# Performance work log

Measured on AMD Instinct MI355X. Metric: run time of the kernel, lower is better.

The kernel has to match this reference:

```python
import jax, jax.numpy as jnp
import numpy as np
from jax import lax

C, NH, HC, HID, P = 192, 8, 64, 512, 16
B, H, W = 2, 128, 128
EPS = 1e-5


def setup_inputs() -> dict:
    key = jax.random.key(0)
    ks = jax.random.split(key, 12)
    f = lambda i, shape: jax.random.normal(ks[i], shape, jnp.float32) * 0.05
    return dict(
        x=jax.random.normal(ks[0], (B, C, H, W), jnp.float32),
        ln1_g=jnp.ones((C,), jnp.float32), ln1_b=jnp.zeros((C,), jnp.float32),
        wq=f(1, (HID, C)), wk=f(2, (HID, C)), wv=f(3, (HID, C)),
        wo=f(4, (C, HID)), bo=jnp.zeros((C,), jnp.float32),
        dw_w=f(5, (C, 1, 3, 3)), dw_b=jnp.zeros((C,), jnp.float32),
        mlp_w=f(6, (C, 2 * C)), mlp_b=jnp.zeros((C,), jnp.float32),
        ln2_g=jnp.ones((C,), jnp.float32), ln2_b=jnp.zeros((C,), jnp.float32),
        c1_w=f(7, (C, C)), c1_b=jnp.zeros((C,), jnp.float32),
        res_w=f(8, (C, 1, 3, 3)), res_b=jnp.zeros((C,), jnp.float32),
        c2_w=f(9, (C, C)), c2_b=jnp.zeros((C,), jnp.float32),
    )


def ln_ch(x, g, b):
    # LayerNorm over the channel dim of an NCHW tensor (biased variance, like torch)
    m = x.mean(1, keepdims=True)
    v = ((x - m) ** 2).mean(1, keepdims=True)
    return (x - m) / jnp.sqrt(v + EPS) * g[None, :, None, None] + b[None, :, None, None]


def inorm(x):
    # InstanceNorm2d, affine=False
    m = x.mean((2, 3), keepdims=True)
    v = ((x - m) ** 2).mean((2, 3), keepdims=True)
    return (x - m) / jnp.sqrt(v + EPS)


def conv1x1(x, w, b=None):
    y = jnp.einsum('oc,bchw->bohw', w, x)
    return y if b is None else y + b[None, :, None, None]


def dwconv(x, w, b):
    y = lax.conv_general_dilated(x, w, (1, 1), 'SAME',
                                 feature_group_count=x.shape[1],
                                 dimension_numbers=('NCHW', 'OIHW', 'NCHW'))
    return y + b[None, :, None, None]


def res_block(x, w, b):
    return jax.nn.gelu(inorm(dwconv(x, w, b)), approximate=False) + x


def dpsa(x, ln_g, ln_b, wq, wk, wv, wo, bo):
    Bs, _, Hs, Ws = x.shape
    xn = ln_ch(x, ln_g, ln_b)

    def proj(w):  # -> (B*NH, H, W, HC)
        t = jnp.einsum('oc,bchw->bohw', w, xn)
        return t.reshape(Bs * NH, HC, Hs, Ws).transpose(0, 2, 3, 1)

    l2n = lambda t: t / jnp.maximum(jnp.linalg.norm(t, axis=-1, keepdims=True), 1e-12)
    q = l2n(proj(wq))
    k = l2n(proj(wk))
    v = proj(wv)

    qs = q.sum((1, 2))                                   # (BH, HC)
    h_scores = jnp.einsum('bc,bhc->bh', qs, k.sum(2))    # (BH, H)
    w_scores = jnp.einsum('bc,bwc->bw', qs, k.sum(1))    # (BH, W)
    _, h_idx = lax.top_k(h_scores, P)
    _, w_idx = lax.top_k(w_scores, P)

    k = jnp.take_along_axis(k, h_idx[:, :, None, None], axis=1)   # (BH, P, W, HC)
    v = jnp.take_along_axis(v, h_idx[:, :, None, None], axis=1)
    k = jnp.take_along_axis(k, w_idx[:, None, :, None], axis=2)   # (BH, P, P, HC)
    v = jnp.take_along_axis(v, w_idx[:, None, :, None], axis=2)

    qf = q.reshape(Bs * NH, Hs * Ws, HC)
    kf = k.reshape(Bs * NH, P * P, HC)
    vf = v.reshape(Bs * NH, P * P, HC)
    attn = jax.nn.softmax(jnp.einsum('bqc,bkc->bqk', qf, kf), axis=-1)
    out = jnp.einsum('bqk,bkc->bqc', attn, vf)
    out = out.reshape(Bs, NH, Hs, Ws, HC).transpose(0, 1, 4, 2, 3).reshape(Bs, NH * HC, Hs, Ws)
    return conv1x1(out, wo, bo)


def reference(x, ln1_g, ln1_b, wq, wk, wv, wo, bo, dw_w, dw_b, mlp_w, mlp_b,
              ln2_g, ln2_b, c1_w, c1_b, res_w, res_b, c2_w, c2_b):
    global_branch = dpsa(x, ln1_g, ln1_b, wq, wk, wv, wo, bo)
    local_branch = dwconv(x, dw_w, dw_b)
    f = jnp.concatenate((local_branch, global_branch), axis=1)
    f = conv1x1(f, mlp_w, mlp_b) + x
    y = ln_ch(f, ln2_g, ln2_b)
    y = jax.nn.gelu(inorm(conv1x1(y, c1_w, c1_b)), approximate=False)
    y = res_block(y, res_w, res_b)
    y = inorm(conv1x1(y, c2_w, c2_b))
    return y
```

## Files before the change

### kernel.cpp

```cpp
#include <hip/hip_runtime.h>
#include <math.h>

constexpr int kC   = 192;
constexpr int kNH  = 8;
constexpr int kHC  = 64;
constexpr int kHID = 512;
constexpr int kP   = 16;
constexpr int kB   = 2;
constexpr int kH   = 128;
constexpr int kW   = 128;
constexpr int kHW  = kH * kW;
constexpr int kN   = kB * kHW;
constexpr float kEPS = 1e-5f;

typedef __attribute__((ext_vector_type(8))) short bf16x8;
typedef __attribute__((ext_vector_type(4))) float f32x4;

__device__ inline unsigned short f2bf(float f) {
    unsigned int u = __builtin_bit_cast(unsigned int, f);
    unsigned int r = (u + 0x7FFFu + ((u >> 16) & 1u)) >> 16;
    return (unsigned short)r;
}
__device__ inline float bf2f(unsigned short u) {
    return __builtin_bit_cast(float, (unsigned int)u << 16);
}
__device__ inline unsigned int cvtpk(float lo, float hi) {
    unsigned int r;
    asm("v_cvt_pk_bf16_f32 %0, %1, %2" : "=v"(r) : "v"(lo), "v"(hi));
    return r;
}
__device__ inline unsigned long long pk4(float a, float b, float c, float d) {
    return (unsigned long long)cvtpk(a, b) | ((unsigned long long)cvtpk(c, d) << 32);
}
__device__ inline f32x4 ubf4(unsigned long long u) {
    f32x4 r;
    r[0] = bf2f((unsigned short)u);
    r[1] = bf2f((unsigned short)(u >> 16));
    r[2] = bf2f((unsigned short)(u >> 32));
    r[3] = bf2f((unsigned short)(u >> 48));
    return r;
}
__device__ inline float gelu_f(float x) {
    return 0.5f * x * (1.0f + erff(x * 0.70710678118654752f));
}

__global__ void prep_kernel(float* __restrict__ zbase,
                            const float* wq, const float* wk, const float* wm,
                            const float* c1, const float* c2,
                            const float* wo, const float* mlp_b, const float* bo,
                            unsigned short* wqb, unsigned short* wkb,
                            unsigned short* mlpb1, unsigned short* c1b, unsigned short* c2b,
                            unsigned short* w2pb, float* bp2)
{
    int i = blockIdx.x * 256 + threadIdx.x;
    if (i < 2304) { zbase[i] = 0.f; return; }
    i -= 2304;
    if (i < 98304) { wqb[i] = f2bf(wq[i]); return; }
    i -= 98304;
    if (i < 98304) { wkb[i] = f2bf(wk[i]); return; }
    i -= 98304;
    if (i < 36864) { int o = i / 192, k = i - o * 192; mlpb1[i] = f2bf(wm[o * 384 + k]); return; }
    i -= 36864;
    if (i < 36864) { c1b[i] = f2bf(c1[i]); return; }
    i -= 36864;
    if (i < 36864) { c2b[i] = f2bf(c2[i]); return; }
    i -= 36864;
    if (i < 98304) {
        int o = i >> 9, j = i & 511;
        const float* a = wm + o * 384 + 192;
        float s = 0.f;
        for (int c = 0; c < 192; ++c) s += a[c] * wo[c * 512 + j];
        w2pb[o * 512 + j] = f2bf(s);
        if (j == 0) {
            float t = mlp_b[o];
            for (int c = 0; c < 192; ++c) t += a[c] * bo[c];
            bp2[o] = t;
        }
    }
}

__global__ __launch_bounds__(256) void txln_kernel(const float* __restrict__ x,
                                                   unsigned short* __restrict__ xpb,
                                                   unsigned short* __restrict__ xnb,
                                                   const float* __restrict__ g,
                                                   const float* __restrict__ bb)
{
    __shared__ float tile[192][65];
    __shared__ float red[2][4][64];
    __shared__ float pms[64], prs[64];
    int hw0 = blockIdx.x * 64;
    int b   = blockIdx.y;
    int tid = threadIdx.x;
    for (int i = tid; i < 192 * 64; i += 256) {
        int c = i >> 6, p = i & 63;
        tile[c][p] = x[(size_t)(b * kC + c) * kHW + hw0 + p];
    }
    __syncthreads();
    {
        int p = tid & 63, qt = tid >> 6;
        float s = 0.f, ss = 0.f;
        for (int c = qt * 48; c < qt * 48 + 48; ++c) {
            float v = tile[c][p]; s += v; ss += v * v;
        }
        red[0][qt][p] = s; red[1][qt][p] = ss;
    }
    __syncthreads();
    if (tid < 64) {
        float s  = red[0][0][tid] + red[0][1][tid] + red[0][2][tid] + red[0][3][tid];
        float ss = red[1][0][tid] + red[1][1][tid] + red[1][2][tid] + red[1][3][tid];
        float m = s * (1.0f / kC);
        float var = ss * (1.0f / kC) - m * m;
        pms[tid] = m;
        prs[tid] = rsqrtf(var + kEPS);
    }
    __syncthreads();
    for (int i = tid; i < 64 * 192; i += 256) {
        int p = i / 192, c = i - p * 192;
        float raw = tile[c][p];
        size_t oi = (size_t)(b * kHW + hw0 + p) * kC + c;
        xpb[oi] = f2bf(raw);
        xnb[oi] = f2bf((raw - pms[p]) * prs[p] * g[c] + bb[c]);
    }
}

__global__ void ln_pm_bf16_kernel(const unsigned short* __restrict__ in,
                                  unsigned short* __restrict__ out,
                                  const float* __restrict__ g, const float* __restrict__ bb)
{
    int t = blockIdx.x * 256 + threadIdx.x;
    int n = t >> 2, q = t & 3;
    const unsigned long long* ip = (const unsigned long long*)(in + (size_t)n * kC) + q * 12;
    f32x4 v[12];
    float s = 0.f, ss = 0.f;
#pragma unroll
    for (int r = 0; r < 12; ++r) {
        v[r] = ubf4(ip[r]);
        s  += (v[r][0] + v[r][1]) + (v[r][2] + v[r][3]);
        ss += (v[r][0]*v[r][0] + v[r][1]*v[r][1]) + (v[r][2]*v[r][2] + v[r][3]*v[r][3]);
    }
    s  += __shfl_xor(s, 1);  s  += __shfl_xor(s, 2);
    ss += __shfl_xor(ss, 1); ss += __shfl_xor(ss, 2);
    float m  = s * (1.0f / kC);
    float var = ss * (1.0f / kC) - m * m;
    float rs = rsqrtf(var + kEPS);
    unsigned long long* op = (unsigned long long*)(out + (size_t)n * kC) + q * 12;
#pragma unroll
    for (int r = 0; r < 12; ++r) {
        f32x4 gg = *(const f32x4*)(g + q * 48 + r * 4);
        f32x4 bv = *(const f32x4*)(bb + q * 48 + r * 4);
        op[r] = pk4((v[r][0]-m)*rs*gg[0] + bv[0], (v[r][1]-m)*rs*gg[1] + bv[1],
                    (v[r][2]-m)*rs*gg[2] + bv[2], (v[r][3]-m)*rs*gg[3] + bv[3]);
    }
}

#define MGEMM_CORE(KVAL, APTR, BPTR)                                              \
    {                                                                             \
        const unsigned short* Ap = APTR;                                          \
        const unsigned short* Bp = BPTR;                                          \
        _Pragma("unroll 2")                                                       \
        for (int k = 0; k < KVAL; k += 32) {                                      \
            bf16x8 a0 = *(const bf16x8*)(Ap + k);                                 \
            bf16x8 a1 = *(const bf16x8*)(Ap + (size_t)16 * KVAL + k);             \
            bf16x8 b0 = *(const bf16x8*)(Bp + k);                                 \
            bf16x8 b1 = *(const bf16x8*)(Bp + (size_t)16 * KVAL + k);             \
            bf16x8 b2 = *(const bf16x8*)(Bp + (size_t)32 * KVAL + k);             \
            bf16x8 b3 = *(const bf16x8*)(Bp + (size_t)48 * KVAL + k);             \
            acc[0][0] = __builtin_amdgcn_mfma_f32_16x16x32_bf16(a0, b0, acc[0][0], 0, 0, 0); \
            acc[0][1] = __builtin_amdgcn_mfma_f32_16x16x32_bf16(a0, b1, acc[0][1], 0, 0, 0); \
            acc[0][2] = __builtin_amdgcn_mfma_f32_16x16x32_bf16(a0, b2, acc[0][2], 0, 0, 0); \
            acc[0][3] = __builtin_amdgcn_mfma_f32_16x16x32_bf16(a0, b3, acc[0][3], 0, 0, 0); \
            acc[1][0] = __builtin_amdgcn_mfma_f32_16x16x32_bf16(a1, b0, acc[1][0], 0, 0, 0); \
            acc[1][1] = __builtin_amdgcn_mfma_f32_16x16x32_bf16(a1, b1, acc[1][1], 0, 0, 0); \
            acc[1][2] = __builtin_amdgcn_mfma_f32_16x16x32_bf16(a1, b2, acc[1][2], 0, 0, 0); \
            acc[1][3] = __builtin_amdgcn_mfma_f32_16x16x32_bf16(a1, b3, acc[1][3], 0, 0, 0); \
        }                                                                         \
    }

__global__ __launch_bounds__(256) void qk_proj_kernel(
    const unsigned short* __restrict__ wqb, const unsigned short* __restrict__ wkb,
    const unsigned short* __restrict__ xnb,
    unsigned short* __restrict__ qpb, unsigned short* __restrict__ kpb,
    float* __restrict__ qpart, float* __restrict__ ksum_h)
{
    __shared__ float rbuf[2][2][4][4][4];
    int nB = blockIdx.x * 128;
    int hp = blockIdx.y;
    const unsigned short* A = blockIdx.z ? wkb : wqb;
    unsigned short* out = blockIdx.z ? kpb : qpb;
    float* red_out = blockIdx.z ? ksum_h : qpart;

    int w = threadIdx.x >> 6, lane = threadIdx.x & 63;
    int l15 = lane & 15, g = lane >> 4;
    int wm = w & 1, wn = w >> 1;
    int oB = hp * 128;

    const unsigned short* Ap = A + (size_t)(oB + wm * 64 + l15) * 192 + 8 * g;
    const unsigned short* Bp = xnb + (size_t)(nB + wn * 64 + l15) * 192 + 8 * g;

    f32x4 acc[4][4];
#pragma unroll
    for (int mt = 0; mt < 4; ++mt)
#pragma unroll
        for (int nt = 0; nt < 4; ++nt) acc[mt][nt] = (f32x4){0.f,0.f,0.f,0.f};

#pragma unroll 2
    for (int k = 0; k < 192; k += 32) {
        bf16x8 a[4], bb[4];
#pragma unroll
        for (int mt = 0; mt < 4; ++mt) a[mt] = *(const bf16x8*)(Ap + (size_t)mt * 16 * 192 + k);
#pragma unroll
        for (int nt = 0; nt < 4; ++nt) bb[nt] = *(const bf16x8*)(Bp + (size_t)nt * 16 * 192 + k);
#pragma unroll
        for (int mt = 0; mt < 4; ++mt)
#pragma unroll
            for (int nt = 0; nt < 4; ++nt)
                acc[mt][nt] = __builtin_amdgcn_mfma_f32_16x16x32_bf16(a[mt], bb[nt], acc[mt][nt], 0, 0, 0);
    }

    float sc[4];
#pragma unroll
    for (int nt = 0; nt < 4; ++nt) {
        float s = 0.f;
#pragma unroll
        for (int mt = 0; mt < 4; ++mt) {
            f32x4 a = acc[mt][nt];
            s += (a[0]*a[0] + a[1]*a[1]) + (a[2]*a[2] + a[3]*a[3]);
        }
        s += __shfl_xor(s, 16);
        s += __shfl_xor(s, 32);
        sc[nt] = 1.0f / fmaxf(sqrtf(s), 1e-12f);
    }

#pragma unroll
    for (int nt = 0; nt < 4; ++nt) {
        int n = nB + wn * 64 + nt * 16 + l15;
#pragma unroll
        for (int mt = 0; mt < 4; ++mt) {
            int o = oB + wm * 64 + mt * 16 + 4 * g;
            f32x4 v = acc[mt][nt];
            *(unsigned long long*)(out + (size_t)n * kHID + o) =
                pk4(v[0]*sc[nt], v[1]*sc[nt], v[2]*sc[nt], v[3]*sc[nt]);
        }
    }

    float sred[4][4] = {};
#pragma unroll
    for (int nt = 0; nt < 4; ++nt)
#pragma unroll
        for (int mt = 0; mt < 4; ++mt) {
            f32x4 a = acc[mt][nt];
            sred[mt][0] += a[0] * sc[nt];
            sred[mt][1] += a[1] * sc[nt];
            sred[mt][2] += a[2] * sc[nt];
            sred[mt][3] += a[3] * sc[nt];
        }
#pragma unroll
    for (int off = 1; off < 16; off <<= 1)
#pragma unroll
        for (int mt = 0; mt < 4; ++mt)
#pragma unroll
            for (int r = 0; r < 4; ++r)
                sred[mt][r] += __shfl_xor(sred[mt][r], off);
    if (l15 == 0)
#pragma unroll
        for (int mt = 0; mt < 4; ++mt)
#pragma unroll
            for (int r = 0; r < 4; ++r)
                rbuf[wm][wn][g][mt][r] = sred[mt][r];
    __syncthreads();
    if (threadIdx.x < 128) {
        int wm2 = threadIdx.x >> 6;
        int o = threadIdx.x & 63;
        int mt2 = o >> 4, g2 = (o >> 2) & 3, r2 = o & 3;
        float v = rbuf[wm2][0][g2][mt2][r2] + rbuf[wm2][1][g2][mt2][r2];
        int row = (nB & (kHW - 1)) >> 7;
        int b = nB >> 14;
        int bh = b * 8 + hp * 2 + wm2;
        red_out[((size_t)(bh * 128 + row)) * 64 + o] = v;
    }
}

__global__ void dwconv_pm_kernel(const unsigned short* __restrict__ in,
                                 unsigned short* __restrict__ out,
                                 const float* __restrict__ wt, const float* __restrict__ bias)
{
    int idx = blockIdx.x * 256 + threadIdx.x;
    int n = idx / 48;
    int c0 = (idx - n * 48) * 4;
    int hw = n & (kHW - 1);
    int h = hw >> 7, ww = hw & 127;
    f32x4 s = *(const f32x4*)(bias + c0);
#pragma unroll
    for (int dy = -1; dy <= 1; ++dy) {
        int hh = h + dy;
        if (hh < 0 || hh >= kH) continue;
#pragma unroll
        for (int dx = -1; dx <= 1; ++dx) {
            int wx = ww + dx;
            if (wx < 0 || wx >= kW) continue;
            f32x4 v = ubf4(*(const unsigned long long*)(in + (size_t)(n + dy * kW + dx) * kC + c0));
            int t = (dy + 1) * 3 + (dx + 1);
            s[0] += v[0] * wt[(c0 + 0) * 9 + t];
            s[1] += v[1] * wt[(c0 + 1) * 9 + t];
            s[2] += v[2] * wt[(c0 + 2) * 9 + t];
            s[3] += v[3] * wt[(c0 + 3) * 9 + t];
        }
    }
    *(unsigned long long*)(out + (size_t)n * kC + c0) = pk4(s[0], s[1], s[2], s[3]);
}

__global__ void sum_h_kernel(const unsigned short* __restrict__ buf, float* __restrict__ out)
{
    __shared__ float red[4][64];
    int w = blockIdx.x, bh = blockIdx.y;
    int hc = threadIdx.x & 63, seg = threadIdx.x >> 6;
    int b = bh >> 3, nh = bh & 7;
    const unsigned short* p = buf + (size_t)(b * kHW + seg * 32 * kW + w) * kHID + nh * kHC + hc;
    float s = 0.f;
    for (int h = 0; h < 32; ++h) s += bf2f(p[(size_t)h * kW * kHID]);
    red[seg][hc] = s;
    __syncthreads();
    if (threadIdx.x < 64)
        out[((size_t)bh * kW + w) * kHC + threadIdx.x] =
            red[0][threadIdx.x] + red[1][threadIdx.x] + red[2][threadIdx.x] + red[3][threadIdx.x];
}

__global__ __launch_bounds__(256) void mgemm_is_kernel(
    const unsigned short* __restrict__ A, const unsigned short* __restrict__ B,
    unsigned short* __restrict__ out, const float* __restrict__ bias,
    float* __restrict__ accp)
{
    __shared__ float sa[2][64], qa[2][64];
    int nB = blockIdx.x * 128, oB = blockIdx.y * 64;
    int w = threadIdx.x >> 6, lane = threadIdx.x & 63;
    int l15 = lane & 15, g = lane >> 4;
    int wm = w & 1, wn = w >> 1;

    f32x4 acc[2][4];
#pragma unroll
    for (int mt = 0; mt < 2; ++mt)
#pragma unroll
        for (int nt = 0; nt < 4; ++nt) acc[mt][nt] = (f32x4){0.f,0.f,0.f,0.f};

    MGEMM_CORE(192, A + (size_t)(oB + wm * 32 + l15) * 192 + 8 * g,
                    B + (size_t)(nB + wn * 64 + l15) * 192 + 8 * g);

    f32x4 vv[2][4];
#pragma unroll
    for (int mt = 0; mt < 2; ++mt)
#pragma unroll
        for (int nt = 0; nt < 4; ++nt) {
            int o = oB + wm * 32 + mt * 16 + 4 * g;
            int n = nB + wn * 64 + nt * 16 + l15;
            f32x4 v = acc[mt][nt] + *(const f32x4*)(bias + o);
            vv[mt][nt] = v;
            *(unsigned long long*)(out + (size_t)n * kC + o) = pk4(v[0], v[1], v[2], v[3]);
        }
    float s2[2][4] = {}, q2[2][4] = {};
#pragma unroll
    for (int mt = 0; mt < 2; ++mt)
#pragma unroll
        for (int nt = 0; nt < 4; ++nt)
#pragma unroll
            for (int r = 0; r < 4; ++r) {
                float v = vv[mt][nt][r];
                s2[mt][r] += v; q2[mt][r] += v * v;
            }
#pragma unroll
    for (int off = 1; off < 16; off <<= 1)
#pragma unroll
        for (int mt = 0; mt < 2; ++mt)
#pragma unroll
            for (int r = 0; r < 4; ++r) {
                s2[mt][r] += __shfl_xor(s2[mt][r], off);
                q2[mt][r] += __shfl_xor(q2[mt][r], off);
            }
    if (l15 == 0)
#pragma unroll
        for (int mt = 0; mt < 2; ++mt)
#pragma unroll
            for (int r = 0; r < 4; ++r) {
                int ol = wm * 32 + mt * 16 + 4 * g + r;
                sa[wn][ol] = s2[mt][r];
                qa[wn][ol] = q2[mt][r];
            }
    __syncthreads();
    if (threadIdx.x < 128) {
        int ol = threadIdx.x & 63, st = threadIdx.x >> 6;
        float v = st ? (qa[0][ol] + qa[1][ol]) : (sa[0][ol] + sa[1][ol]);
        int b = nB >> 14;
        atomicAdd(&accp[(size_t)(b * kC + oB + ol) * 2 + st], v);
    }
}

__global__ __launch_bounds__(256) void mgemm_mlp_kernel(
    const unsigned short* __restrict__ A1, const unsigned short* __restrict__ B1,
    const unsigned short* __restrict__ A2, const unsigned short* __restrict__ B2,
    unsigned short* __restrict__ out, const float* __restrict__ bp2,
    const unsigned short* __restrict__ res)
{
    int nB = blockIdx.x * 128, oB = blockIdx.y * 64;
    int w = threadIdx.x >> 6, lane = threadIdx.x & 63;
    int l15 = lane & 15, g = lane >> 4;
    int wm = w & 1, wn = w >> 1;

    f32x4 acc[2][4];
#pragma unroll
    for (int mt = 0; mt < 2; ++mt)
#pragma unroll
        for (int nt = 0; nt < 4; ++nt) acc[mt][nt] = (f32x4){0.f,0.f,0.f,0.f};

    MGEMM_CORE(192, A1 + (size_t)(oB + wm * 32 + l15) * 192 + 8 * g,
                    B1 + (size_t)(nB + wn * 64 + l15) * 192 + 8 * g);
    MGEMM_CORE(512, A2 + (size_t)(oB + wm * 32 + l15) * 512 + 8 * g,
                    B2 + (size_t)(nB + wn * 64 + l15) * 512 + 8 * g);

#pragma unroll
    for (int mt = 0; mt < 2; ++mt)
#pragma unroll
        for (int nt = 0; nt < 4; ++nt) {
            int o = oB + wm * 32 + mt * 16 + 4 * g;
            int n = nB + wn * 64 + nt * 16 + l15;
            f32x4 v = acc[mt][nt];
            v[0] += bp2[o]; v[1] += bp2[o+1]; v[2] += bp2[o+2]; v[3] += bp2[o+3];
            v += ubf4(*(const unsigned long long*)(res + (size_t)n * kC + o));
            *(unsigned long long*)(out + (size_t)n * kC + o) = pk4(v[0], v[1], v[2], v[3]);
        }
}

__global__ void score_topk_kernel(const float* __restrict__ qpart,
                                  const float* __restrict__ ksum_h,
                                  const float* __restrict__ ksum_w,
                                  int* __restrict__ hidx, int* __restrict__ widx)
{
    __shared__ float qsl[2][64];
    __shared__ float hs[128], ws[128];
    int bh = blockIdx.x;
    int tid = threadIdx.x;
    int hc = tid & 63, grp = tid >> 6;
    {
        const float* qp = qpart + ((size_t)bh * 128 + grp * 64) * 64 + hc;
        float s = 0.f;
        for (int i = 0; i < 64; ++i) s += qp[(size_t)i * 64];
        qsl[grp][hc] = s;
    }
    __syncthreads();
    if (tid < 64) qsl[0][tid] += qsl[1][tid];
    __syncthreads();
    {
        const float* kh = ksum_h + ((size_t)bh * 128 + tid) * 64;
        const float* kw = ksum_w + ((size_t)bh * 128 + tid) * 64;
        float sh = 0.f, sw = 0.f;
        for (int c = 0; c < 64; ++c) {
            float q = qsl[0][c];
            sh += q * kh[c];
            sw += q * kw[c];
        }
        hs[tid] = sh; ws[tid] = sw;
    }
    __syncthreads();
    int sel = tid >> 6;
    const float* sc = sel ? ws : hs;
    int* out = (sel ? widx : hidx) + bh * kP;
    int lane = tid & 63;
    float v0 = sc[lane], v1 = sc[lane + 64];
    int i0 = lane, i1 = lane + 64;
    for (int p = 0; p < kP; ++p) {
        float bv; int bi;
        if (v1 > v0) { bv = v1; bi = i1; } else { bv = v0; bi = i0; }
#pragma unroll
        for (int off = 1; off < 64; off <<= 1) {
            float ov = __shfl_xor(bv, off);
            int   oi = __shfl_xor(bi, off);
            if (ov > bv || (ov == bv && oi < bi)) { bv = ov; bi = oi; }
        }
        if (lane == 0) out[p] = bi;
        if (i0 == bi) v0 = -INFINITY;
        if (i1 == bi) v1 = -INFINITY;
    }
}

__global__ void gather_kv_kernel(const unsigned short* __restrict__ kpb,
                                 const unsigned short* __restrict__ xnb,
                                 const float* __restrict__ wv,
                                 const int* __restrict__ hidx, const int* __restrict__ widx,
                                 unsigned short* __restrict__ kf, unsigned short* __restrict__ vfT)
{
    int bh = blockIdx.y, p1 = blockIdx.x;
    int b = bh >> 3, nh = bh & 7;
    int hc = threadIdx.x & 63, pg = threadIdx.x >> 6;
    int hrow = hidx[bh * kP + p1];
    int o = nh * kHC + hc;
    const float* wvp = wv + (size_t)o * kC;
    for (int p2 = pg; p2 < kP; p2 += 4) {
        int wcol = widx[bh * kP + p2];
        int n = b * kHW + hrow * kW + wcol;
        int kidx = p1 * kP + p2;
        kf[((size_t)bh * 256 + kidx) * 64 + hc] = kpb[(size_t)n * kHID + nh * kHC + hc];
        const unsigned int* xr = (const unsigned int*)(xnb + (size_t)n * kC);
        float s = 0.f;
        for (int c2 = 0; c2 < kC / 2; ++c2) {
            unsigned int u = xr[c2];
            s += wvp[c2 * 2]     * bf2f((unsigned short)(u & 0xffff));
            s += wvp[c2 * 2 + 1] * bf2f((unsigned short)(u >> 16));
        }
        vfT[((size_t)bh * 64 + hc) * 256 + kidx] = f2bf(s);
    }
}

__global__ __launch_bounds__(256) void attn_kernel(
    const unsigned short* __restrict__ qpb, unsigned short* __restrict__ ob,
    const unsigned short* __restrict__ kf, const unsigned short* __restrict__ vfT)
{
    __shared__ unsigned short pls[64 * 256];
    __shared__ float lred[4][4][16];

    int bh = blockIdx.y; int b = bh >> 3, nh = bh & 7;
    int nbase = b * kHW + blockIdx.x * 128;
    int tid = threadIdx.x;
    int w = tid >> 6, lane = tid & 63, l15 = lane & 15, g = lane >> 4;

    const unsigned short* kfb = kf + (size_t)bh * 256 * 64;
    bf16x8 ak[4][2];
#pragma unroll
    for (int mt = 0; mt < 4; ++mt)
#pragma unroll
        for (int kt = 0; kt < 2; ++kt)
            ak[mt][kt] = *(const bf16x8*)&kfb[(size_t)(w * 64 + mt * 16 + l15) * 64 + kt * 32 + 8 * g];

    const unsigned short* vfb = vfT + (size_t)bh * 64 * 256;

#pragma unroll
    for (int sub = 0; sub < 2; ++sub) {
        int n0 = nbase + sub * 64;
        bf16x8 bq[4][2];
#pragma unroll
        for (int nt = 0; nt < 4; ++nt)
#pragma unroll
            for (int kt = 0; kt < 2; ++kt)
                bq[nt][kt] = *(const bf16x8*)(qpb + (size_t)(n0 + nt * 16 + l15) * kHID
                                              + nh * kHC + kt * 32 + 8 * g);

        f32x4 acc[4][4];
#pragma unroll
        for (int mt = 0; mt < 4; ++mt)
#pragma unroll
            for (int nt = 0; nt < 4; ++nt) acc[mt][nt] = (f32x4){0.f,0.f,0.f,0.f};

#pragma unroll
        for (int kt = 0; kt < 2; ++kt)
#pragma unroll
            for (int mt = 0; mt < 4; ++mt)
#pragma unroll
                for (int nt = 0; nt < 4; ++nt)
                    acc[mt][nt] = __builtin_amdgcn_mfma_f32_16x16x32_bf16(
                        ak[mt][kt], bq[nt][kt], acc[mt][nt], 0, 0, 0);

        if (sub) __syncthreads();

        float lpart[4] = {0.f, 0.f, 0.f, 0.f};
#pragma unroll
        for (int mt = 0; mt < 4; ++mt)
#pragma unroll
            for (int nt = 0; nt < 4; ++nt) {
                float e0 = __expf(acc[mt][nt][0]);
                float e1 = __expf(acc[mt][nt][1]);
                float e2 = __expf(acc[mt][nt][2]);
                float e3 = __expf(acc[mt][nt][3]);
                lpart[nt] += (e0 + e1) + (e2 + e3);
                int qq = nt * 16 + l15;
                int k0 = w * 64 + mt * 16 + 4 * g;
                int kx = k0 ^ ((qq & 7) << 3);
                *(unsigned long long*)&pls[qq * 256 + kx] = pk4(e0, e1, e2, e3);
            }
#pragma unroll
        for (int nt = 0; nt < 4; ++nt) {
            lpart[nt] += __shfl_xor(lpart[nt], 16);
            lpart[nt] += __shfl_xor(lpart[nt], 32);
        }
        if (g == 0)
#pragma unroll
            for (int nt = 0; nt < 4; ++nt) lred[w][nt][l15] = lpart[nt];
        __syncthreads();

        f32x4 oacc[4];
#pragma unroll
        for (int nt = 0; nt < 4; ++nt) oacc[nt] = (f32x4){0.f,0.f,0.f,0.f};

#pragma unroll
        for (int ks = 0; ks < 8; ++ks) {
            bf16x8 av = *(const bf16x8*)&vfb[(size_t)(w * 16 + l15) * 256 + ks * 32 + 8 * g];
#pragma unroll
            for (int nt = 0; nt < 4; ++nt) {
                int qq = nt * 16 + l15;
                int kx = (ks * 32 + 8 * g) ^ ((qq & 7) << 3);
                bf16x8 bp = *(const bf16x8*)&pls[qq * 256 + kx];
                oacc[nt] = __builtin_amdgcn_mfma_f32_16x16x32_bf16(av, bp, oacc[nt], 0, 0, 0);
            }
        }

#pragma unroll
        for (int nt = 0; nt < 4; ++nt) {
            float l = lred[0][nt][l15] + lred[1][nt][l15] + lred[2][nt][l15] + lred[3][nt][l15];
            float inv = 1.0f / l;
            int qq = nt * 16 + l15;
            int hc0 = w * 16 + 4 * g;
            *(unsigned long long*)(ob + (size_t)(n0 + qq) * kHID + nh * kHC + hc0) =
                pk4(oacc[nt][0] * inv, oacc[nt][1] * inv, oacc[nt][2] * inv, oacc[nt][3] * inv);
        }
    }
}

__global__ void istats_bf16_kernel(const unsigned short* __restrict__ in, float* __restrict__ acc)
{
    int n0 = blockIdx.x * 64;
    int b = n0 >> 14;
    int c = threadIdx.x;
    float s = 0.f, ss = 0.f;
    for (int p = 0; p < 64; ++p) {
        float v = bf2f(in[(size_t)(n0 + p) * kC + c]);
        s += v; ss += v * v;
    }
    atomicAdd(&acc[(size_t)(b * kC + c) * 2],     s);
    atomicAdd(&acc[(size_t)(b * kC + c) * 2 + 1], ss);
}

__device__ inline void inorm_ms(const float* acc, int b, int c, float& m, float& rs)
{
    float s  = acc[(size_t)(b * kC + c) * 2];
    float ss = acc[(size_t)(b * kC + c) * 2 + 1];
    m = s * (1.0f / kHW);
    float var = ss * (1.0f / kHW) - m * m;
    rs = rsqrtf(var + kEPS);
}

template<int MODE>
__global__ void apply_pm_kernel(const unsigned short* __restrict__ in, const float* __restrict__ acc,
                                unsigned short* __restrict__ out, const unsigned short* __restrict__ addsrc)
{
    int idx = blockIdx.x * 256 + threadIdx.x;
    int n = idx / 48;
    int c0 = (idx - n * 48) * 4;
    int b = n >> 14;
    f32x4 v = ubf4(*(const unsigned long long*)(in + (size_t)n * kC + c0));
    f32x4 r;
#pragma unroll
    for (int j = 0; j < 4; ++j) {
        float m, rs;
        inorm_ms(acc, b, c0 + j, m, rs);
        float x = (v[j] - m) * rs;
        r[j] = gelu_f(x);
    }
    if (MODE == 1)
        r += ubf4(*(const unsigned long long*)(addsrc + (size_t)n * kC + c0));
    *(unsigned long long*)(out + (size_t)n * kC + c0) = pk4(r[0], r[1], r[2], r[3]);
}

__global__ __launch_bounds__(256) void final_kernel(const unsigned short* __restrict__ in,
                                                    const float* __restrict__ acc,
                                                    float* __restrict__ out)
{
    __shared__ unsigned short tile[192][68];
    int n0 = blockIdx.x * 64;
    int b = n0 >> 14;
    int hw0 = n0 & (kHW - 1);
    int tid = threadIdx.x;
    for (int i = tid; i < 64 * 48; i += 256) {
        int p = i / 48, cq = i - p * 48;
        unsigned long long u = *(const unsigned long long*)(in + (size_t)(n0 + p) * kC + cq * 4);
        tile[cq * 4 + 0][p] = (unsigned short)u;
        tile[cq * 4 + 1][p] = (unsigned short)(u >> 16);
        tile[cq * 4 + 2][p] = (unsigned short)(u >> 32);
        tile[cq * 4 + 3][p] = (unsigned short)(u >> 48);
    }
    __syncthreads();
    for (int i = tid; i < 192 * 16; i += 256) {
        int c = i >> 4, grp = i & 15;
        float m, rs;
        inorm_ms(acc, b, c, m, rs);
        f32x4 o;
#pragma unroll
        for (int j = 0; j < 4; ++j)
            o[j] = (bf2f(tile[c][grp * 4 + j]) - m) * rs;
        *(f32x4*)(out + (size_t)(b * kC + c) * kHW + hw0 + grp * 4) = o;
    }
}

extern "C" void kernel_launch(void* const* d_in, const int* in_sizes, int n_in,
                              void* d_out, int out_size, void* d_ws, size_t ws_size,
                              hipStream_t stream)
{
    const float* x     = (const float*)d_in[0];
    const float* ln1_g = (const float*)d_in[1];
    const float* ln1_b = (const float*)d_in[2];
    const float* wq    = (const float*)d_in[3];
    const float* wk    = (const float*)d_in[4];
    const float* wv    = (const float*)d_in[5];
    const float* wo    = (const float*)d_in[6];
    const float* bo    = (const float*)d_in[7];
    const float* dw_w  = (const float*)d_in[8];
    const float* dw_b  = (const float*)d_in[9];
    const float* mlp_w = (const float*)d_in[10];
    const float* mlp_b = (const float*)d_in[11];
    const float* ln2_g = (const float*)d_in[12];
    const float* ln2_b = (const float*)d_in[13];
    const float* c1_w  = (const float*)d_in[14];
    const float* c1_b  = (const float*)d_in[15];
    const float* res_w = (const float*)d_in[16];
    const float* res_b = (const float*)d_in[17];
    const float* c2_w  = (const float*)d_in[18];
    const float* c2_b  = (const float*)d_in[19];

    char* base = (char*)d_ws;
    unsigned short* XPb = (unsigned short*)(base);
    unsigned short* XNb = (unsigned short*)(base + 25165824);
    unsigned short* QPb = (unsigned short*)(base + 37748736);
    unsigned short* F   = QPb;
    unsigned short* T2  = QPb;
    unsigned short* KPb = (unsigned short*)(base + 71303168);
    unsigned short* OB  = KPb;
    unsigned short* Y2  = KPb;
    unsigned short* LB  = (unsigned short*)(base + 104857600);
    unsigned short* Y3  = LB;
    unsigned short* T1  = (unsigned short*)(base + 117440512);
    unsigned short* R   = T1;
    char* sm = base + 130023424;
    float* qpart  = (float*)(sm);                 sm += 524288;
    float* ksum_h = (float*)(sm);                 sm += 524288;
    float* ksum_w = (float*)(sm);                 sm += 524288;
    float* acc0   = (float*)(sm);                 sm += 3072;
    float* acc1   = (float*)(sm);                 sm += 3072;
    float* acc2   = (float*)(sm);                 sm += 3072;
    unsigned short* kf   = (unsigned short*)(sm); sm += 524288;
    unsigned short* vfT  = (unsigned short*)(sm); sm += 524288;
    unsigned short* wqb  = (unsigned short*)(sm); sm += 196608;
    unsigned short* wkb  = (unsigned short*)(sm); sm += 196608;
    unsigned short* mlpb1= (unsigned short*)(sm); sm += 73728;
    unsigned short* c1b  = (unsigned short*)(sm); sm += 73728;
    unsigned short* c2b  = (unsigned short*)(sm); sm += 73728;
    unsigned short* w2pb = (unsigned short*)(sm); sm += 196608;
    float* bp2 = (float*)(sm);                    sm += 1024;
    int* hidx = (int*)(sm);                       sm += 1024;
    int* widx = (int*)(sm);

    prep_kernel<<<1593, 256, 0, stream>>>(acc0, wq, wk, mlp_w, c1_w, c2_w,
                                          wo, mlp_b, bo,
                                          wqb, wkb, mlpb1, c1b, c2b, w2pb, bp2);
    txln_kernel<<<dim3(kHW / 64, kB), 256, 0, stream>>>(x, XPb, XNb, ln1_g, ln1_b);
    qk_proj_kernel<<<dim3(kN / 128, 4, 2), 256, 0, stream>>>(wqb, wkb, XNb, QPb, KPb,
                                                             qpart, ksum_h);
    dwconv_pm_kernel<<<(kN * 48) / 256, 256, 0, stream>>>(XPb, LB, dw_w, dw_b);
    sum_h_kernel<<<dim3(kW, 16), 256, 0, stream>>>(KPb, ksum_w);
    score_topk_kernel<<<16, 128, 0, stream>>>(qpart, ksum_h, ksum_w, hidx, widx);
    gather_kv_kernel<<<dim3(kP, 16), 256, 0, stream>>>(KPb, XNb, wv, hidx, widx, kf, vfT);
    attn_kernel<<<dim3(kHW / 128, 16), 256, 0, stream>>>(QPb, OB, kf, vfT);
    mgemm_mlp_kernel<<<dim3(kN / 128, kC / 64), 256, 0, stream>>>(mlpb1, LB, w2pb, OB, F, bp2, XPb);
    ln_pm_bf16_kernel<<<(kN * 4) / 256, 256, 0, stream>>>(F, XNb, ln2_g, ln2_b);
    mgemm_is_kernel<<<dim3(kN / 128, kC / 64), 256, 0, stream>>>(c1b, XNb, T1, c1_b, acc0);
    apply_pm_kernel<0><<<(kN * 48) / 256, 256, 0, stream>>>(T1, acc0, Y2, nullptr);
    dwconv_pm_kernel<<<(kN * 48) / 256, 256, 0, stream>>>(Y2, R, res_w, res_b);
    istats_bf16_kernel<<<kN / 64, 192, 0, stream>>>(R, acc1);
    apply_pm_kernel<1><<<(kN * 48) / 256, 256, 0, stream>>>(R, acc1, Y3, Y2);
    mgemm_is_kernel<<<dim3(kN / 128, kC / 64), 256, 0, stream>>>(c2b, Y3, T2, c2_b, acc2);
    final_kernel<<<kN / 64, 256, 0, stream>>>(T2, acc2, (float*)d_out);
}
```

Before: 462.6 us.

## Fuse channel LayerNorm into MLP GEMM epilogue and merge QK projection with dwconv

The MLP GEMM now computes all 192 output channels per 128-pixel block, using 6 waves and 384 threads. This lets it reduce the per-pixel LayerNorm statistics in shared memory and write the normalized bf16 output directly, which removes the separate ln_pm kernel and the round trip through the intermediate F buffer. Separately, the QK projection and the first depthwise conv are merged into one launch that dispatches on block index. The changes cut launches and global memory traffic, but the GEMM now uses more registers (16 accumulators per wave), launches fewer blocks, and lets divergent block types share one kernel's register allocation.

```diff
diff --git a/kernel.cpp b/kernel.cpp
--- a/kernel.cpp
+++ b/kernel.cpp
@@ -123,36 +123,6 @@
     }
 }
 
-__global__ void ln_pm_bf16_kernel(const unsigned short* __restrict__ in,
-                                  unsigned short* __restrict__ out,
-                                  const float* __restrict__ g, const float* __restrict__ bb)
-{
-    int t = blockIdx.x * 256 + threadIdx.x;
-    int n = t >> 2, q = t & 3;
-    const unsigned long long* ip = (const unsigned long long*)(in + (size_t)n * kC) + q * 12;
-    f32x4 v[12];
-    float s = 0.f, ss = 0.f;
-#pragma unroll
-    for (int r = 0; r < 12; ++r) {
-        v[r] = ubf4(ip[r]);
-        s  += (v[r][0] + v[r][1]) + (v[r][2] + v[r][3]);
-        ss += (v[r][0]*v[r][0] + v[r][1]*v[r][1]) + (v[r][2]*v[r][2] + v[r][3]*v[r][3]);
-    }
-    s  += __shfl_xor(s, 1);  s  += __shfl_xor(s, 2);
-    ss += __shfl_xor(ss, 1); ss += __shfl_xor(ss, 2);
-    float m  = s * (1.0f / kC);
-    float var = ss * (1.0f / kC) - m * m;
-    float rs = rsqrtf(var + kEPS);
-    unsigned long long* op = (unsigned long long*)(out + (size_t)n * kC) + q * 12;
-#pragma unroll
-    for (int r = 0; r < 12; ++r) {
-        f32x4 gg = *(const f32x4*)(g + q * 48 + r * 4);
-        f32x4 bv = *(const f32x4*)(bb + q * 48 + r * 4);
-        op[r] = pk4((v[r][0]-m)*rs*gg[0] + bv[0], (v[r][1]-m)*rs*gg[1] + bv[1],
-                    (v[r][2]-m)*rs*gg[2] + bv[2], (v[r][3]-m)*rs*gg[3] + bv[3]);
-    }
-}
-
 #define MGEMM_CORE(KVAL, APTR, BPTR)                                              \
     {                                                                             \
         const unsigned short* Ap = APTR;                                          \
@@ -176,18 +146,19 @@
         }                                                                         \
     }
 
-__global__ __launch_bounds__(256) void qk_proj_kernel(
-    const unsigned short* __restrict__ wqb, const unsigned short* __restrict__ wkb,
-    const unsigned short* __restrict__ xnb,
-    unsigned short* __restrict__ qpb, unsigned short* __restrict__ kpb,
-    float* __restrict__ qpart, float* __restrict__ ksum_h)
+__device__ void qk_proj_body(int nblk, int hp, int isK,
+                             const unsigned short* __restrict__ wqb,
+                             const unsigned short* __restrict__ wkb,
+                             const unsigned short* __restrict__ xnb,
+                             unsigned short* __restrict__ qpb,
+                             unsigned short* __restrict__ kpb,
+                             float* __restrict__ qpart, float* __restrict__ ksum_h)
 {
     __shared__ float rbuf[2][2][4][4][4];
-    int nB = blockIdx.x * 128;
-    int hp = blockIdx.y;
-    const unsigned short* A = blockIdx.z ? wkb : wqb;
-    unsigned short* out = blockIdx.z ? kpb : qpb;
-    float* red_out = blockIdx.z ? ksum_h : qpart;
+    int nB = nblk * 128;
+    const unsigned short* A = isK ? wkb : wqb;
+    unsigned short* out = isK ? kpb : qpb;
+    float* red_out = isK ? ksum_h : qpart;
 
     int w = threadIdx.x >> 6, lane = threadIdx.x & 63;
     int l15 = lane & 15, g = lane >> 4;
@@ -280,11 +251,10 @@
     }
 }
 
-__global__ void dwconv_pm_kernel(const unsigned short* __restrict__ in,
-                                 unsigned short* __restrict__ out,
-                                 const float* __restrict__ wt, const float* __restrict__ bias)
-{
-    int idx = blockIdx.x * 256 + threadIdx.x;
+__device__ void dwconv_body(int idx, const unsigned short* __restrict__ in,
+                            unsigned short* __restrict__ out,
+                            const float* __restrict__ wt, const float* __restrict__ bias)
+{
     int n = idx / 48;
     int c0 = (idx - n * 48) * 4;
     int hw = n & (kHW - 1);
@@ -309,6 +279,23 @@
     *(unsigned long long*)(out + (size_t)n * kC + c0) = pk4(s[0], s[1], s[2], s[3]);
 }
 
+__global__ __launch_bounds__(256) void qkdw_kernel(
+    const unsigned short* __restrict__ wqb, const unsigned short* __restrict__ wkb,
+    const unsigned short* __restrict__ xnb, const unsigned short* __restrict__ xpb,
+    unsigned short* __restrict__ qpb, unsigned short* __restrict__ kpb,
+    float* __restrict__ qpart, float* __restrict__ ksum_h,
+    unsigned short* __restrict__ lb,
+    const float* __restrict__ dw_w, const float* __restrict__ dw_b)
+{
+    int id = blockIdx.x;
+    if (id < 2048) {
+        qk_proj_body(id & 255, (id >> 8) & 3, id >> 10, wqb, wkb, xnb,
+                     qpb, kpb, qpart, ksum_h);
+    } else {
+        dwconv_body((id - 2048) * 256 + threadIdx.x, xpb, lb, dw_w, dw_b);
+    }
+}
+
 __global__ void sum_h_kernel(const unsigned short* __restrict__ buf, float* __restrict__ out)
 {
     __shared__ float red[4][64];
@@ -393,39 +380,110 @@
     }
 }
 
-__global__ __launch_bounds__(256) void mgemm_mlp_kernel(
+__global__ __launch_bounds__(384) void mgemm_mlp_ln_kernel(
     const unsigned short* __restrict__ A1, const unsigned short* __restrict__ B1,
     const unsigned short* __restrict__ A2, const unsigned short* __restrict__ B2,
     unsigned short* __restrict__ out, const float* __restrict__ bp2,
-    const unsigned short* __restrict__ res)
-{
-    int nB = blockIdx.x * 128, oB = blockIdx.y * 64;
+    const unsigned short* __restrict__ res,
+    const float* __restrict__ lng, const float* __restrict__ lnb)
+{
+    __shared__ float lnS[3][2][4][16], lnQ[3][2][4][16];
+    int nB = blockIdx.x * 128;
     int w = threadIdx.x >> 6, lane = threadIdx.x & 63;
     int l15 = lane & 15, g = lane >> 4;
-    int wm = w & 1, wn = w >> 1;
-
-    f32x4 acc[2][4];
-#pragma unroll
-    for (int mt = 0; mt < 2; ++mt)
+    int om = w >> 1, on = w & 1;
+    int oB = om * 64;
+
+    f32x4 acc[4][4];
+#pragma unroll
+    for (int mt = 0; mt < 4; ++mt)
 #pragma unroll
         for (int nt = 0; nt < 4; ++nt) acc[mt][nt] = (f32x4){0.f,0.f,0.f,0.f};
 
-    MGEMM_CORE(192, A1 + (size_t)(oB + wm * 32 + l15) * 192 + 8 * g,
-                    B1 + (size_t)(nB + wn * 64 + l15) * 192 + 8 * g);
-    MGEMM_CORE(512, A2 + (size_t)(oB + wm * 32 + l15) * 512 + 8 * g,
-                    B2 + (size_t)(nB + wn * 64 + l15) * 512 + 8 * g);
-
-#pragma unroll
-    for (int mt = 0; mt < 2; ++mt)
-#pragma unroll
-        for (int nt = 0; nt < 4; ++nt) {
-            int o = oB + wm * 32 + mt * 16 + 4 * g;
-            int n = nB + wn * 64 + nt * 16 + l15;
+    {
+        const unsigned short* Ap = A1 + (size_t)(oB + l15) * 192 + 8 * g;
+        const unsigned short* Bp = B1 + (size_t)(nB + on * 64 + l15) * 192 + 8 * g;
+#pragma unroll 2
+        for (int k = 0; k < 192; k += 32) {
+            bf16x8 a[4], bb[4];
+#pragma unroll
+            for (int mt = 0; mt < 4; ++mt) a[mt] = *(const bf16x8*)(Ap + (size_t)mt * 16 * 192 + k);
+#pragma unroll
+            for (int nt = 0; nt < 4; ++nt) bb[nt] = *(const bf16x8*)(Bp + (size_t)nt * 16 * 192 + k);
+#pragma unroll
+            for (int mt = 0; mt < 4; ++mt)
+#pragma unroll
+                for (int nt = 0; nt < 4; ++nt)
+                    acc[mt][nt] = __builtin_amdgcn_mfma_f32_16x16x32_bf16(a[mt], bb[nt], acc[mt][nt], 0, 0, 0);
+        }
+    }
+    {
+        const unsigned short* Ap = A2 + (size_t)(oB + l15) * 512 + 8 * g;
+        const unsigned short* Bp = B2 + (size_t)(nB + on * 64 + l15) * 512 + 8 * g;
+#pragma unroll 2
+        for (int k = 0; k < 512; k += 32) {
+            bf16x8 a[4], bb[4];
+#pragma unroll
+            for (int mt = 0; mt < 4; ++mt) a[mt] = *(const bf16x8*)(Ap + (size_t)mt * 16 * 512 + k);
+#pragma unroll
+            for (int nt = 0; nt < 4; ++nt) bb[nt] = *(const bf16x8*)(Bp + (size_t)nt * 16 * 512 + k);
+#pragma unroll
+            for (int mt = 0; mt < 4; ++mt)
+#pragma unroll
+                for (int nt = 0; nt < 4; ++nt)
+                    acc[mt][nt] = __builtin_amdgcn_mfma_f32_16x16x32_bf16(a[mt], bb[nt], acc[mt][nt], 0, 0, 0);
+        }
+    }
+
+    float sp[4] = {}, sq[4] = {};
+#pragma unroll
+    for (int nt = 0; nt < 4; ++nt) {
+        int n = nB + on * 64 + nt * 16 + l15;
+#pragma unroll
+        for (int mt = 0; mt < 4; ++mt) {
+            int o = oB + mt * 16 + 4 * g;
             f32x4 v = acc[mt][nt];
             v[0] += bp2[o]; v[1] += bp2[o+1]; v[2] += bp2[o+2]; v[3] += bp2[o+3];
             v += ubf4(*(const unsigned long long*)(res + (size_t)n * kC + o));
-            *(unsigned long long*)(out + (size_t)n * kC + o) = pk4(v[0], v[1], v[2], v[3]);
-        }
+            acc[mt][nt] = v;
+            sp[nt] += (v[0] + v[1]) + (v[2] + v[3]);
+            sq[nt] += (v[0]*v[0] + v[1]*v[1]) + (v[2]*v[2] + v[3]*v[3]);
+        }
+    }
+#pragma unroll
+    for (int nt = 0; nt < 4; ++nt) {
+        sp[nt] += __shfl_xor(sp[nt], 16);
+        sp[nt] += __shfl_xor(sp[nt], 32);
+        sq[nt] += __shfl_xor(sq[nt], 16);
+        sq[nt] += __shfl_xor(sq[nt], 32);
+    }
+    if (g == 0)
+#pragma unroll
+        for (int nt = 0; nt < 4; ++nt) {
+            lnS[om][on][nt][l15] = sp[nt];
+            lnQ[om][on][nt][l15] = sq[nt];
+        }
+    __syncthreads();
+
+#pragma unroll
+    for (int nt = 0; nt < 4; ++nt) {
+        float S = lnS[0][on][nt][l15] + lnS[1][on][nt][l15] + lnS[2][on][nt][l15];
+        float Q = lnQ[0][on][nt][l15] + lnQ[1][on][nt][l15] + lnQ[2][on][nt][l15];
+        float m = S * (1.0f / kC);
+        float var = Q * (1.0f / kC) - m * m;
+        float rs = rsqrtf(var + kEPS);
+        int n = nB + on * 64 + nt * 16 + l15;
+#pragma unroll
+        for (int mt = 0; mt < 4; ++mt) {
+            int o = oB + mt * 16 + 4 * g;
+            f32x4 v = acc[mt][nt];
+            f32x4 gg = *(const f32x4*)(lng + o);
+            f32x4 bv = *(const f32x4*)(lnb + o);
+            *(unsigned long long*)(out + (size_t)n * kC + o) =
+                pk4((v[0]-m)*rs*gg[0] + bv[0], (v[1]-m)*rs*gg[1] + bv[1],
+                    (v[2]-m)*rs*gg[2] + bv[2], (v[3]-m)*rs*gg[3] + bv[3]);
+        }
+    }
 }
 
 __global__ void score_topk_kernel(const float* __restrict__ qpart,
@@ -609,6 +667,13 @@
                 pk4(oacc[nt][0] * inv, oacc[nt][1] * inv, oacc[nt][2] * inv, oacc[nt][3] * inv);
         }
     }
+}
+
+__global__ void dwconv_pm_kernel(const unsigned short* __restrict__ in,
+                                 unsigned short* __restrict__ out,
+                                 const float* __restrict__ wt, const float* __restrict__ bias)
+{
+    dwconv_body(blockIdx.x * 256 + threadIdx.x, in, out, wt, bias);
 }
 
 __global__ void istats_bf16_kernel(const unsigned short* __restrict__ in, float* __restrict__ acc)
@@ -715,7 +780,6 @@
     unsigned short* XPb = (unsigned short*)(base);
     unsigned short* XNb = (unsigned short*)(base + 25165824);
     unsigned short* QPb = (unsigned short*)(base + 37748736);
-    unsigned short* F   = QPb;
     unsigned short* T2  = QPb;
     unsigned short* KPb = (unsigned short*)(base + 71303168);
     unsigned short* OB  = KPb;
@@ -747,15 +811,14 @@
                                           wo, mlp_b, bo,
                                           wqb, wkb, mlpb1, c1b, c2b, w2pb, bp2);
     txln_kernel<<<dim3(kHW / 64, kB), 256, 0, stream>>>(x, XPb, XNb, ln1_g, ln1_b);
-    qk_proj_kernel<<<dim3(kN / 128, 4, 2), 256, 0, stream>>>(wqb, wkb, XNb, QPb, KPb,
-                                                             qpart, ksum_h);
-    dwconv_pm_kernel<<<(kN * 48) / 256, 256, 0, stream>>>(XPb, LB, dw_w, dw_b);
+    qkdw_kernel<<<8192, 256, 0, stream>>>(wqb, wkb, XNb, XPb, QPb, KPb,
+                                          qpart, ksum_h, LB, dw_w, dw_b);
     sum_h_kernel<<<dim3(kW, 16), 256, 0, stream>>>(KPb, ksum_w);
     score_topk_kernel<<<16, 128, 0, stream>>>(qpart, ksum_h, ksum_w, hidx, widx);
     gather_kv_kernel<<<dim3(kP, 16), 256, 0, stream>>>(KPb, XNb, wv, hidx, widx, kf, vfT);
     attn_kernel<<<dim3(kHW / 128, 16), 256, 0, stream>>>(QPb, OB, kf, vfT);
-    mgemm_mlp_kernel<<<dim3(kN / 128, kC / 64), 256, 0, stream>>>(mlpb1, LB, w2pb, OB, F, bp2, XPb);
-    ln_pm_bf16_kernel<<<(kN * 4) / 256, 256, 0, stream>>>(F, XNb, ln2_g, ln2_b);
+    mgemm_mlp_ln_kernel<<<kN / 128, 384, 0, stream>>>(mlpb1, LB, w2pb, OB, XNb, bp2, XPb,
+                                                      ln2_g, ln2_b);
     mgemm_is_kernel<<<dim3(kN / 128, kC / 64), 256, 0, stream>>>(c1b, XNb, T1, c1_b, acc0);
     apply_pm_kernel<0><<<(kN * 48) / 256, 256, 0, stream>>>(T1, acc0, Y2, nullptr);
     dwconv_pm_kernel<<<(kN * 48) / 256, 256, 0, stream>>>(Y2, R, res_w, res_b);
```

After: 451.8 us. -2.3%, faster.
